# Kernel tuning notes

Hardware: AMD Instinct MI355X
Metric: run time of the kernel (lower is better)

Reference implementation:

```python
import jax, jax.numpy as jnp
import numpy as np

DXV, DRUGV = 10000, 3000
DXANC, DRUGANC = 2000, 600
A = 8            # max ancestors per leaf
ONTOD = 128; EHRD = 128; ATTND = 128; PTATTND = 128; DPL = 500
B, T, DXN, DRUGN = 64, 20, 30, 30


def _l2norm(x):
    n = jnp.sqrt(jnp.sum(x * x, axis=-1, keepdims=True))
    return x / jnp.maximum(n, 1e-12)


def _onto_emb(emb, leaves, ancestors, aW, ab, cW, cb):
    # GRAM-style ontology attention: per leaf, attend over its ancestor set.
    le = emb[leaves]          # (V, A, ONTOD)
    ae = emb[ancestors]       # (V, A, ONTOD)
    s = jnp.tanh(jnp.concatenate([le, ae], -1) @ aW + ab) @ cW + cb  # (V, A, 1)
    attn = jax.nn.softmax(s, axis=1)
    out = jnp.sum(attn * ae, axis=1)                                 # (V, ONTOD)
    pad = jnp.zeros((1, out.shape[1]), out.dtype)                    # padding row at idx V
    return jnp.concatenate([out, pad], axis=0)


def setup_inputs() -> dict:
    key = jax.random.key(0)
    ks = jax.random.split(key, 24)
    s = 0.02
    dxseqs = jax.random.randint(ks[0], (B, T, DXN), 0, DXV + 1)
    drugseqs = jax.random.randint(ks[1], (B, T, DRUGN), 0, DRUGV + 1)
    dx_onehot = jax.random.uniform(ks[2], (T, B, DXV), dtype=jnp.float32)
    drug_onehot = jax.random.uniform(ks[3], (T, B, DRUGV), dtype=jnp.float32)
    dx_leaves = jnp.broadcast_to(jnp.arange(DXV)[:, None], (DXV, A))
    dx_ancestors = jax.random.randint(ks[4], (DXV, A), 0, DXV + DXANC).at[:, 0].set(jnp.arange(DXV))
    drug_leaves = jnp.broadcast_to(jnp.arange(DRUGV)[:, None], (DRUGV, A))
    drug_ancestors = jax.random.randint(ks[5], (DRUGV, A), 0, DRUGV + DRUGANC).at[:, 0].set(jnp.arange(DRUGV))
    ehr_dx_emb = (jax.random.normal(ks[6], (DXV + 1, EHRD)) * s).at[DXV].set(0.0)
    ehr_drug_emb = (jax.random.normal(ks[7], (DRUGV + 1, EHRD)) * s).at[DRUGV].set(0.0)
    return {
        "dxseqs": dxseqs, "drugseqs": drugseqs,
        "dx_onehot": dx_onehot, "drug_onehot": drug_onehot,
        "dx_leaves": dx_leaves, "dx_ancestors": dx_ancestors,
        "drug_leaves": drug_leaves, "drug_ancestors": drug_ancestors,
        "dx_onto_emb": jax.random.normal(ks[8], (DXV + DXANC, ONTOD)) * s,
        "dx_onto_aW": jax.random.normal(ks[9], (2 * ONTOD, ATTND)) * s,
        "dx_onto_ab": jnp.zeros((ATTND,)),
        "dx_onto_cW": jax.random.normal(ks[10], (ATTND, 1)) * s,
        "dx_onto_cb": jnp.zeros((1,)),
        "drug_onto_emb": jax.random.normal(ks[11], (DRUGV + DRUGANC, ONTOD)) * s,
        "drug_onto_aW": jax.random.normal(ks[12], (2 * ONTOD, ATTND)) * s,
        "drug_onto_ab": jnp.zeros((ATTND,)),
        "drug_onto_cW": jax.random.normal(ks[13], (ATTND, 1)) * s,
        "drug_onto_cb": jnp.zeros((1,)),
        "ehr_dx_emb": ehr_dx_emb, "ehr_drug_emb": ehr_drug_emb,
        "co_W": jax.random.normal(ks[14], (EHRD, DXV + DRUGV)) * s,
        "co_b": jnp.zeros((DXV + DRUGV,)),
        "attn_W": jax.random.normal(ks[15], (2 * ONTOD + 2 * EHRD, PTATTND)) * s,
        "attn_b": jnp.zeros((PTATTND,)),
        "comb_W": jax.random.normal(ks[16], (PTATTND, 1)) * s,
        "comb_b": jnp.zeros((1,)),
        "dp_W": jax.random.normal(ks[17], (ONTOD + EHRD, DPL)) * s,
        "dp_b": jnp.zeros((DPL,)),
        "read_W": jax.random.normal(ks[18], (ONTOD + EHRD, 1)) * s,
        "read_b": jnp.zeros((1,)),
    }


def reference(dxseqs, drugseqs, dx_onehot, drug_onehot,
              dx_leaves, dx_ancestors, drug_leaves, drug_ancestors,
              dx_onto_emb, dx_onto_aW, dx_onto_ab, dx_onto_cW, dx_onto_cb,
              drug_onto_emb, drug_onto_aW, drug_onto_ab, drug_onto_cW, drug_onto_cb,
              ehr_dx_emb, ehr_drug_emb, co_W, co_b,
              attn_W, attn_b, comb_W, comb_b, dp_W, dp_b, read_W, read_b):
    dxALL = _onto_emb(dx_onto_emb, dx_leaves, dx_ancestors, dx_onto_aW, dx_onto_ab, dx_onto_cW, dx_onto_cb)      # (DXV+1, ONTOD)
    drugALL = _onto_emb(drug_onto_emb, drug_leaves, drug_ancestors, drug_onto_aW, drug_onto_ab, drug_onto_cW, drug_onto_cb)
    dxE = ehr_dx_emb[dxseqs]                                # (B,T,DXN,EHRD)
    drugE = ehr_drug_emb[drugseqs]                          # (B,T,DRUGN,EHRD)
    EHREmb = jnp.concatenate([dxE, drugE], axis=2)          # (B,T,N,EHRD)
    ontoEmb = jnp.concatenate([dxALL[dxseqs], drugALL[drugseqs]], axis=2)  # (B,T,N,ONTOD)
    EHRVEmb = _l2norm(jnp.sum(dxE, axis=2)) + _l2norm(jnp.sum(drugE, axis=2))  # (B,T,EHRD)
    dxontoV = jnp.einsum('tbv,vd->btd', dx_onehot, dxALL[:-1])
    drugontoV = jnp.einsum('tbv,vd->btd', drug_onehot, drugALL[:-1])
    cooccurU = jax.nn.softmax(EHRVEmb @ co_W + co_b, axis=2)               # (B,T,DXV+DRUGV)
    vonehot = jnp.concatenate([jnp.transpose(dx_onehot, (1, 0, 2)),
                               jnp.transpose(drug_onehot, (1, 0, 2))], axis=2)
    cooccur_loss = -jnp.mean(jnp.sum(vonehot * jnp.log(cooccurU), axis=(1, 2)))
    ontoV = _l2norm(dxontoV) + _l2norm(drugontoV)
    vs = jnp.concatenate([ontoV, EHRVEmb], axis=2)          # (B,T,ONTOD+EHRD)
    dxdrug = jnp.concatenate([EHREmb, ontoEmb], axis=3)     # (B,T,N,EHRD+ONTOD)
    N = dxdrug.shape[2]
    vs_rep = jnp.broadcast_to(vs[:, :, None, :], (vs.shape[0], vs.shape[1], N, vs.shape[2]))
    attnInput = jnp.concatenate([vs_rep, dxdrug], axis=3)   # (B,T,N,2*ONTOD+2*EHRD)
    pre = jnp.tanh(attnInput @ attn_W + attn_b) @ comb_W + comb_b          # (B,T,N,1)
    attn = jax.nn.softmax(pre, axis=2)
    vs2 = jnp.sum(attn * dxdrug, axis=2)                    # (B,T,EHRD+ONTOD)
    vs_dp = _l2norm(vs2)
    DP_result = jax.nn.softmax(jnp.tanh(vs_dp) @ dp_W + dp_b, axis=2)
    read_result = jax.nn.sigmoid(vs_dp @ read_W + read_b)
    return (read_result, DP_result, cooccur_loss * 10.0)
```

## Files before the change

kernel.cpp:

```cpp
#include <hip/hip_runtime.h>
#include <hip/hip_bf16.h>
#include <math.h>

#define BB 64
#define TT 20
#define BT 1280
#define DXV 10000
#define DRUGV 3000
#define COV 13000
#define DPL 500
#define KC 40

typedef __attribute__((ext_vector_type(8))) short short8v;
typedef __attribute__((ext_vector_type(4))) float f32x4;

__device__ __forceinline__ unsigned short f2bf(float f) {
  __hip_bfloat16 h = __float2bfloat16(f);
  return *reinterpret_cast<unsigned short*>(&h);
}

__global__ __launch_bounds__(256, 4) void k_onto(
    const float* __restrict__ emb, const int* __restrict__ leaves, const int* __restrict__ anc,
    const float* __restrict__ aW, const float* __restrict__ ab, const float* __restrict__ cW,
    float* __restrict__ out)
{
  __shared__ __align__(16) float xe[4][128];
  __shared__ __align__(16) float xa[4][8][128];
  __shared__ float part[4][8][2];
  __shared__ float sv[32];
  const int tid = threadIdx.x;
  const int v0 = blockIdx.x * 4;

  for (int i = tid; i < 4*128; i += 256) {
    const int lv = i >> 7, d = i & 127;
    xe[lv][d] = emb[leaves[(v0 + lv)*8] * 128 + d];
  }
  for (int i = tid; i < 32*128; i += 256) {
    const int row = i >> 7, d = i & 127;
    xa[row >> 3][row & 7][d] = emb[anc[(v0 + (row >> 3))*8 + (row & 7)] * 128 + d];
  }
  __syncthreads();

  const int j = tid & 127, half = tid >> 7;

  float ld[4];
  { const float abj = ab[j]; ld[0] = ld[1] = ld[2] = ld[3] = abj; }
  for (int k0 = 0; k0 < 128; k0 += 4) {
    const float w0 = aW[(k0+0)*128 + j];
    const float w1 = aW[(k0+1)*128 + j];
    const float w2 = aW[(k0+2)*128 + j];
    const float w3 = aW[(k0+3)*128 + j];
    #pragma unroll
    for (int lv = 0; lv < 4; ++lv) {
      const float4 x4 = *reinterpret_cast<const float4*>(&xe[lv][k0]);
      ld[lv] = fmaf(x4.x, w0, fmaf(x4.y, w1, fmaf(x4.z, w2, fmaf(x4.w, w3, ld[lv]))));
    }
  }

  float acc[4][4];
  #pragma unroll
  for (int lv = 0; lv < 4; ++lv)
    #pragma unroll
    for (int ai = 0; ai < 4; ++ai) acc[lv][ai] = ld[lv];
  for (int k0 = 0; k0 < 128; k0 += 4) {
    const float w0 = aW[(128+k0+0)*128 + j];
    const float w1 = aW[(128+k0+1)*128 + j];
    const float w2 = aW[(128+k0+2)*128 + j];
    const float w3 = aW[(128+k0+3)*128 + j];
    float4 es[16];
    #pragma unroll
    for (int lv = 0; lv < 4; ++lv)
      #pragma unroll
      for (int ai = 0; ai < 4; ++ai)
        es[lv*4 + ai] = *reinterpret_cast<const float4*>(&xa[lv][half + 2*ai][k0]);
    #pragma unroll
    for (int lv = 0; lv < 4; ++lv)
      #pragma unroll
      for (int ai = 0; ai < 4; ++ai) {
        const float4 e4 = es[lv*4 + ai];
        acc[lv][ai] = fmaf(e4.x, w0, fmaf(e4.y, w1, fmaf(e4.z, w2, fmaf(e4.w, w3, acc[lv][ai]))));
      }
  }

  {
    const float cwj = cW[j];
    #pragma unroll
    for (int lv = 0; lv < 4; ++lv)
      #pragma unroll
      for (int ai = 0; ai < 4; ++ai) {
        float p = tanhf(acc[lv][ai]) * cwj;
        for (int off = 32; off; off >>= 1) p += __shfl_down(p, off);
        if ((tid & 63) == 0) part[lv][half + 2*ai][(tid >> 6) & 1] = p;
      }
  }
  __syncthreads();
  if (tid < 32) sv[tid] = part[tid >> 3][tid & 7][0] + part[tid >> 3][tid & 7][1];
  __syncthreads();
  if (tid < 4) {
    float m = -1e30f;
    #pragma unroll
    for (int a = 0; a < 8; ++a) m = fmaxf(m, sv[tid*8 + a]);
    float e[8], ssum = 0.f;
    #pragma unroll
    for (int a = 0; a < 8; ++a) { e[a] = __expf(sv[tid*8 + a] - m); ssum += e[a]; }
    const float inv = 1.f / ssum;
    #pragma unroll
    for (int a = 0; a < 8; ++a) sv[tid*8 + a] = e[a] * inv;
  }
  __syncthreads();
  #pragma unroll
  for (int it = 0; it < 2; ++it) {
    const int i = it*256 + tid;
    const int lv = i >> 7, d = i & 127;
    float o = 0.f;
    #pragma unroll
    for (int a = 0; a < 8; ++a) o += sv[lv*8 + a] * xa[lv][a][d];
    out[(v0 + lv)*128 + d] = o;
  }
}

__global__ __launch_bounds__(128) void k_ehr(
    const int* __restrict__ dxs, const int* __restrict__ drs,
    const float* __restrict__ edx, const float* __restrict__ edr,
    float* __restrict__ vs)
{
  const int bt = blockIdx.x, d = threadIdx.x;
  float sdx = 0.f, sdr = 0.f;
  for (int n = 0; n < 30; ++n) sdx += edx[dxs[bt*30 + n]*128 + d];
  for (int n = 0; n < 30; ++n) sdr += edr[drs[bt*30 + n]*128 + d];
  __shared__ float red[2][2];
  float p1 = sdx*sdx, p2 = sdr*sdr;
  for (int off = 32; off; off >>= 1) { p1 += __shfl_down(p1, off); p2 += __shfl_down(p2, off); }
  if ((d & 63) == 0) { red[0][d>>6] = p1; red[1][d>>6] = p2; }
  __syncthreads();
  const float n1 = sqrtf(red[0][0] + red[0][1]);
  const float n2 = sqrtf(red[1][0] + red[1][1]);
  vs[bt*256 + 128 + d] = sdx / fmaxf(n1, 1e-12f) + sdr / fmaxf(n2, 1e-12f);
}

__global__ __launch_bounds__(256, 4) void k_einsum(
    const float* __restrict__ oneh, const float* __restrict__ tabl,
    float* __restrict__ outp, int V, int vcount)
{
  __shared__ __align__(16) float As[32][KC];
  __shared__ __align__(16) float Bs[KC][128];
  const int tid = threadIdx.x;
  const int rbase = blockIdx.x * 32;
  const int vbase = blockIdx.y * vcount;
  const int cg = tid & 31, rg = tid >> 5;
  const int d0 = cg * 4, r0 = rg * 4;
  float acc[4][4];
  #pragma unroll
  for (int r = 0; r < 4; ++r)
    #pragma unroll
    for (int q = 0; q < 4; ++q) acc[r][q] = 0.f;

  for (int c0 = 0; c0 < vcount; c0 += KC) {
    __syncthreads();
    for (int i = tid; i < 320; i += 256) {
      const int r = i / 10, q = i % 10;
      const int row = rbase + r;
      const int b = row / TT, t = row % TT;
      *reinterpret_cast<float4*>(&As[r][q*4]) =
          *reinterpret_cast<const float4*>(&oneh[(t*BB + b)*V + vbase + c0 + q*4]);
    }
    for (int i = tid; i < 1280; i += 256) {
      const int rr = i >> 5, q = i & 31;
      *reinterpret_cast<float4*>(&Bs[rr][q*4]) =
          *reinterpret_cast<const float4*>(&tabl[(vbase + c0 + rr)*128 + q*4]);
    }
    __syncthreads();
    #pragma unroll
    for (int kk = 0; kk < KC; kk += 4) {
      const float4 b0 = *reinterpret_cast<const float4*>(&Bs[kk+0][d0]);
      const float4 b1 = *reinterpret_cast<const float4*>(&Bs[kk+1][d0]);
      const float4 b2 = *reinterpret_cast<const float4*>(&Bs[kk+2][d0]);
      const float4 b3 = *reinterpret_cast<const float4*>(&Bs[kk+3][d0]);
      float4 a4[4];
      #pragma unroll
      for (int r = 0; r < 4; ++r) a4[r] = *reinterpret_cast<const float4*>(&As[r0 + r][kk]);
      #pragma unroll
      for (int r = 0; r < 4; ++r) {
        acc[r][0] = fmaf(a4[r].x, b0.x, fmaf(a4[r].y, b1.x, fmaf(a4[r].z, b2.x, fmaf(a4[r].w, b3.x, acc[r][0]))));
        acc[r][1] = fmaf(a4[r].x, b0.y, fmaf(a4[r].y, b1.y, fmaf(a4[r].z, b2.y, fmaf(a4[r].w, b3.y, acc[r][1]))));
        acc[r][2] = fmaf(a4[r].x, b0.z, fmaf(a4[r].y, b1.z, fmaf(a4[r].z, b2.z, fmaf(a4[r].w, b3.z, acc[r][2]))));
        acc[r][3] = fmaf(a4[r].x, b0.w, fmaf(a4[r].y, b1.w, fmaf(a4[r].z, b2.w, fmaf(a4[r].w, b3.w, acc[r][3]))));
      }
    }
  }
  #pragma unroll
  for (int r = 0; r < 4; ++r) {
    const int row = rbase + r0 + r;
    #pragma unroll
    for (int q = 0; q < 4; ++q)
      atomicAdd(&outp[row*128 + d0 + q], acc[r][q]);
  }
}

__global__ __launch_bounds__(128) void k_vs(
    const float* __restrict__ dxo, const float* __restrict__ dro, float* __restrict__ vs)
{
  const int bt = blockIdx.x, d = threadIdx.x;
  const float a = dxo[bt*128 + d], b = dro[bt*128 + d];
  __shared__ float red[2][2];
  float p1 = a*a, p2 = b*b;
  for (int off = 32; off; off >>= 1) { p1 += __shfl_down(p1, off); p2 += __shfl_down(p2, off); }
  if ((d & 63) == 0) { red[0][d>>6] = p1; red[1][d>>6] = p2; }
  __syncthreads();
  const float n1 = sqrtf(red[0][0] + red[0][1]);
  const float n2 = sqrtf(red[1][0] + red[1][1]);
  vs[bt*256 + d] = a / fmaxf(n1, 1e-12f) + b / fmaxf(n2, 1e-12f);
}

__global__ __launch_bounds__(256, 4) void k_cooc(
    const float* __restrict__ vs, const float* __restrict__ coW, const float* __restrict__ cob,
    const float* __restrict__ dxoh, const float* __restrict__ droh,
    float* __restrict__ es_g, float* __restrict__ od_g, float* __restrict__ os_g)
{
  __shared__ __align__(16) float ev[16][128];
  __shared__ float l_es[16], l_od[16], l_os[16];
  const int tid = threadIdx.x;
  const int rbase = blockIdx.x * 16;
  const int cbase = blockIdx.y * 512;
  for (int i = tid; i < 2048; i += 256)
    ev[i >> 7][i & 127] = vs[(rbase + (i >> 7))*256 + 128 + (i & 127)];
  if (tid < 16) { l_es[tid] = 0.f; l_od[tid] = 0.f; l_os[tid] = 0.f; }
  __syncthreads();
  float es[16], od[16], os[16];
  #pragma unroll
  for (int r = 0; r < 16; ++r) { es[r] = 0.f; od[r] = 0.f; os[r] = 0.f; }
  #pragma unroll 1
  for (int vi = 0; vi < 2; ++vi) {
    const int v = cbase + vi*256 + tid;
    if (v < COV) {
      float acc[16];
      #pragma unroll
      for (int r = 0; r < 16; ++r) acc[r] = 0.f;
      for (int k0 = 0; k0 < 128; k0 += 4) {
        const float c0 = coW[(k0+0)*COV + v];
        const float c1 = coW[(k0+1)*COV + v];
        const float c2 = coW[(k0+2)*COV + v];
        const float c3 = coW[(k0+3)*COV + v];
        float4 e4s[16];
        #pragma unroll
        for (int r = 0; r < 16; ++r) e4s[r] = *reinterpret_cast<const float4*>(&ev[r][k0]);
        #pragma unroll
        for (int r = 0; r < 16; ++r)
          acc[r] = fmaf(e4s[r].x, c0, fmaf(e4s[r].y, c1, fmaf(e4s[r].z, c2, fmaf(e4s[r].w, c3, acc[r]))));
      }
      const float cb = cob[v];
      #pragma unroll
      for (int r = 0; r < 16; ++r) {
        const int row = rbase + r;
        const int b = row / TT, t = row % TT;
        const float lgv = acc[r] + cb;
        const float oh = (v < DXV) ? dxoh[(t*BB + b)*DXV + v]
                                   : droh[(t*BB + b)*DRUGV + (v - DXV)];
        es[r] += __expf(lgv);
        od[r] = fmaf(oh, lgv, od[r]);
        os[r] += oh;
      }
    }
  }
  #pragma unroll
  for (int r = 0; r < 16; ++r) {
    float a = es[r], b2 = od[r], c2 = os[r];
    for (int off = 32; off; off >>= 1) {
      a += __shfl_down(a, off); b2 += __shfl_down(b2, off); c2 += __shfl_down(c2, off);
    }
    if ((tid & 63) == 0) { atomicAdd(&l_es[r], a); atomicAdd(&l_od[r], b2); atomicAdd(&l_os[r], c2); }
  }
  __syncthreads();
  if (tid < 16) {
    atomicAdd(&es_g[rbase + tid], l_es[tid]);
    atomicAdd(&od_g[rbase + tid], l_od[tid]);
    atomicAdd(&os_g[rbase + tid], l_os[tid]);
  }
}

__global__ __launch_bounds__(256) void k_loss(
    const float* __restrict__ es_g, const float* __restrict__ od_g, const float* __restrict__ os_g,
    float* __restrict__ out)
{
  const int tid = threadIdx.x;
  float a = 0.f;
  for (int r = tid; r < BT; r += 256)
    a += logf(es_g[r]) * os_g[r] - od_g[r];
  __shared__ float red[4];
  for (int off = 32; off; off >>= 1) a += __shfl_down(a, off);
  if ((tid & 63) == 0) red[tid >> 6] = a;
  __syncthreads();
  if (tid == 0) out[0] = (red[0] + red[1] + red[2] + red[3]) * (10.f / (float)BB);
}

__global__ __launch_bounds__(128) void k_cvtw(
    const float* __restrict__ aW, unsigned short* __restrict__ aWbT)
{
  const int k = blockIdx.x, n = threadIdx.x;
  aWbT[n*256 + k] = f2bf(aW[(256 + k)*128 + n]);
}

__global__ __launch_bounds__(256, 4) void k_attn(
    const int* __restrict__ dxs, const int* __restrict__ drs,
    const float* __restrict__ edx, const float* __restrict__ edr,
    const float* __restrict__ dxALL, const float* __restrict__ drugALL,
    const float* __restrict__ vs, const float* __restrict__ aW,
    const float* __restrict__ ab, const float* __restrict__ cWc,
    const unsigned short* __restrict__ aWbT,
    float* __restrict__ vsdp)
{
  __shared__ __align__(16) unsigned short X2[64*256];
  __shared__ __align__(16) float vrow[256];
  __shared__ float bp[2][128];
  __shared__ float base[128];
  __shared__ float sattn[64];
  __shared__ int codes[60];
  __shared__ float red[4];
  const int tid = threadIdx.x;
  const int bt = blockIdx.x;
  char* x2b = reinterpret_cast<char*>(X2);

  if (tid < 64) sattn[tid] = 0.f;
  if (tid < 60) codes[tid] = (tid < 30) ? dxs[bt*30 + tid] : drs[bt*30 + tid - 30];
  vrow[tid] = vs[bt*256 + tid];
  __syncthreads();

  for (int idx = tid; idx < 60*64; idx += 256) {
    const int n = idx >> 6, q = idx & 63;
    const float* src = (q < 32) ? ((n < 30) ? edx : edr)
                                : ((n < 30) ? dxALL : drugALL);
    const float4 v = *reinterpret_cast<const float4*>(&src[codes[n]*128 + (q & 31)*4]);
    ushort4 h;
    h.x = f2bf(v.x); h.y = f2bf(v.y); h.z = f2bf(v.z); h.w = f2bf(v.w);
    const int byte = (n*512 + q*8) ^ ((n & 7) << 4);
    *reinterpret_cast<ushort4*>(x2b + byte) = h;
  }
  for (int idx = tid; idx < 4*64; idx += 256) {
    const int n = 60 + (idx >> 6), q = idx & 63;
    *reinterpret_cast<ushort4*>(x2b + ((n*512 + q*8) ^ ((n & 7) << 4))) = ushort4{0,0,0,0};
  }

  const int j = tid & 127, ng = tid >> 7;
  {
    float p = 0.f;
    const int kb = ng * 128;
    for (int k0 = 0; k0 < 128; k0 += 4) {
      const float4 v4 = *reinterpret_cast<const float4*>(&vrow[kb + k0]);
      p = fmaf(v4.x, aW[(kb+k0+0)*128 + j],
          fmaf(v4.y, aW[(kb+k0+1)*128 + j],
          fmaf(v4.z, aW[(kb+k0+2)*128 + j],
          fmaf(v4.w, aW[(kb+k0+3)*128 + j], p))));
    }
    bp[ng][j] = p;
  }
  __syncthreads();
  if (tid < 128) base[tid] = ab[tid] + bp[0][tid] + bp[1][tid];
  __syncthreads();

  const int lane = tid & 63, w = tid >> 6;
  const int l15 = lane & 15, kg = lane >> 4;
  f32x4 acc[4][2];
  #pragma unroll
  for (int mt = 0; mt < 4; ++mt)
    #pragma unroll
    for (int ns = 0; ns < 2; ++ns) acc[mt][ns] = f32x4{0.f, 0.f, 0.f, 0.f};

  #pragma unroll
  for (int kt = 0; kt < 8; ++kt) {
    short8v a[4];
    #pragma unroll
    for (int mt = 0; mt < 4; ++mt) {
      const int row = mt*16 + l15;
      const int byte = (row*512 + kt*64 + kg*16) ^ ((row & 7) << 4);
      a[mt] = *reinterpret_cast<const short8v*>(x2b + byte);
    }
    #pragma unroll
    for (int ns = 0; ns < 2; ++ns) {
      const int ncol = (2*w + ns)*16 + l15;
      const short8v b = *reinterpret_cast<const short8v*>(
          reinterpret_cast<const char*>(aWbT) + ncol*512 + kt*64 + kg*16);
      #pragma unroll
      for (int mt = 0; mt < 4; ++mt)
        acc[mt][ns] = __builtin_amdgcn_mfma_f32_16x16x32_bf16(a[mt], b, acc[mt][ns], 0, 0, 0);
    }
  }

  {
    const int c0 = 2*w*16 + l15, c1 = c0 + 16;
    const float b0 = base[c0], b1 = base[c1];
    const float cw0 = cWc[c0], cw1 = cWc[c1];
    #pragma unroll
    for (int mt = 0; mt < 4; ++mt) {
      #pragma unroll
      for (int r = 0; r < 4; ++r) {
        float p = fmaf(cw0, tanhf(b0 + acc[mt][0][r]), cw1 * tanhf(b1 + acc[mt][1][r]));
        p += __shfl_xor(p, 1); p += __shfl_xor(p, 2);
        p += __shfl_xor(p, 4); p += __shfl_xor(p, 8);
        const int row = mt*16 + kg*4 + r;
        if (l15 == 0 && row < 60) atomicAdd(&sattn[row], p);
      }
    }
  }
  __syncthreads();

  if (tid < 64) {
    const float v = (tid < 60) ? sattn[tid] : -1e30f;
    float m = v;
    for (int off = 32; off; off >>= 1) m = fmaxf(m, __shfl_xor(m, off));
    const float e = (tid < 60) ? __expf(v - m) : 0.f;
    float s = e;
    for (int off = 32; off; off >>= 1) s += __shfl_xor(s, off);
    if (tid < 60) sattn[tid] = e / s;
  }
  __syncthreads();

  float acc2 = 0.f;
  {
    const int d2 = tid * 2;
    for (int n = 0; n < 60; ++n) {
      const unsigned short u = *reinterpret_cast<const unsigned short*>(
          x2b + ((n*512 + d2) ^ ((n & 7) << 4)));
      acc2 = fmaf(sattn[n], __uint_as_float(((unsigned)u) << 16), acc2);
    }
  }
  float p = acc2 * acc2;
  for (int off = 32; off; off >>= 1) p += __shfl_down(p, off);
  if ((tid & 63) == 0) red[tid >> 6] = p;
  __syncthreads();
  const float nrm = sqrtf(red[0] + red[1] + red[2] + red[3]);
  vsdp[bt*256 + tid] = acc2 / fmaxf(nrm, 1e-12f);
}

__global__ __launch_bounds__(256) void k_out(
    const float* __restrict__ vsdp, const float* __restrict__ dpW, const float* __restrict__ dpb,
    const float* __restrict__ rW, const float* __restrict__ rb, float* __restrict__ out)
{
  __shared__ __align__(16) float tv[256];
  __shared__ float lg[512];
  __shared__ float red[4], red2[4], red3[4];
  const int bt = blockIdx.x, tid = threadIdx.x;
  const float vraw = vsdp[bt*256 + tid];
  tv[tid] = tanhf(vraw);
  __syncthreads();
  for (int l = tid; l < DPL; l += 256) {
    float a = dpb[l];
    for (int k0 = 0; k0 < 256; k0 += 4) {
      const float4 t4 = *reinterpret_cast<const float4*>(&tv[k0]);
      a = fmaf(t4.x, dpW[(k0+0)*DPL + l],
          fmaf(t4.y, dpW[(k0+1)*DPL + l],
          fmaf(t4.z, dpW[(k0+2)*DPL + l],
          fmaf(t4.w, dpW[(k0+3)*DPL + l], a))));
    }
    lg[l] = a;
  }
  __syncthreads();
  float m = -1e30f;
  for (int l = tid; l < DPL; l += 256) m = fmaxf(m, lg[l]);
  for (int off = 32; off; off >>= 1) m = fmaxf(m, __shfl_xor(m, off));
  if ((tid & 63) == 0) red[tid >> 6] = m;
  __syncthreads();
  m = fmaxf(fmaxf(red[0], red[1]), fmaxf(red[2], red[3]));
  float s = 0.f;
  for (int l = tid; l < DPL; l += 256) s += __expf(lg[l] - m);
  for (int off = 32; off; off >>= 1) s += __shfl_xor(s, off);
  if ((tid & 63) == 0) red2[tid >> 6] = s;
  __syncthreads();
  s = red2[0] + red2[1] + red2[2] + red2[3];
  const float inv = 1.f / s;
  for (int l = tid; l < DPL; l += 256) out[BT + bt*DPL + l] = __expf(lg[l] - m) * inv;
  float p = vraw * rW[tid];
  for (int off = 32; off; off >>= 1) p += __shfl_down(p, off);
  if ((tid & 63) == 0) red3[tid >> 6] = p;
  __syncthreads();
  if (tid == 0) {
    const float tot = red3[0] + red3[1] + red3[2] + red3[3] + rb[0];
    out[bt] = 1.f / (1.f + __expf(-tot));
  }
}

extern "C" void kernel_launch(void* const* d_in, const int* in_sizes, int n_in,
                              void* d_out, int out_size, void* d_ws, size_t ws_size,
                              hipStream_t stream) {
  const int*   dxseqs = (const int*)d_in[0];
  const int*   drseqs = (const int*)d_in[1];
  const float* dxoh   = (const float*)d_in[2];
  const float* droh   = (const float*)d_in[3];
  const int*   dxlv   = (const int*)d_in[4];
  const int*   dxan   = (const int*)d_in[5];
  const int*   drlv   = (const int*)d_in[6];
  const int*   dran   = (const int*)d_in[7];
  const float* dxoe   = (const float*)d_in[8];
  const float* dxaW   = (const float*)d_in[9];
  const float* dxab   = (const float*)d_in[10];
  const float* dxcW   = (const float*)d_in[11];
  const float* droe   = (const float*)d_in[13];
  const float* draW   = (const float*)d_in[14];
  const float* drab   = (const float*)d_in[15];
  const float* drcW   = (const float*)d_in[16];
  const float* edx    = (const float*)d_in[18];
  const float* edr    = (const float*)d_in[19];
  const float* coW    = (const float*)d_in[20];
  const float* cob    = (const float*)d_in[21];
  const float* aW     = (const float*)d_in[22];
  const float* ab     = (const float*)d_in[23];
  const float* cWc    = (const float*)d_in[24];
  const float* dpW    = (const float*)d_in[26];
  const float* dpb    = (const float*)d_in[27];
  const float* rW     = (const float*)d_in[28];
  const float* rb     = (const float*)d_in[29];
  float* out = (float*)d_out;

  float* ws      = (float*)d_ws;
  float* dxALL   = ws;
  float* drugALL = dxALL   + 10001*128;
  float* vsbuf   = drugALL + 3001*128;
  float* dxoV    = vsbuf   + 1280*256;
  float* droV    = dxoV    + 1280*128;
  float* vsdp    = droV    + 1280*128;
  float* es_g    = vsdp    + 1280*256;
  float* od_g    = es_g    + 1280;
  float* os_g    = od_g    + 1280;
  unsigned short* aWbT = (unsigned short*)(os_g + 1280);

  hipMemsetAsync(dxALL + 10000*128, 0, 128*sizeof(float), stream);
  hipMemsetAsync(drugALL + 3000*128, 0, 128*sizeof(float), stream);
  hipMemsetAsync(dxoV, 0, 2*1280*128*sizeof(float), stream);
  hipMemsetAsync(es_g, 0, 3*1280*sizeof(float), stream);

  k_cvtw<<<256, 128, 0, stream>>>(aW, aWbT);
  k_onto<<<DXV/4,  256, 0, stream>>>(dxoe, dxlv, dxan, dxaW, dxab, dxcW, dxALL);
  k_onto<<<DRUGV/4,256, 0, stream>>>(droe, drlv, dran, draW, drab, drcW, drugALL);
  k_ehr<<<BT, 128, 0, stream>>>(dxseqs, drseqs, edx, edr, vsbuf);
  k_einsum<<<dim3(BT/32, 10), 256, 0, stream>>>(dxoh, dxALL, dxoV, DXV, 1000);
  k_einsum<<<dim3(BT/32, 5),  256, 0, stream>>>(droh, drugALL, droV, DRUGV, 600);
  k_vs<<<BT, 128, 0, stream>>>(dxoV, droV, vsbuf);
  k_cooc<<<dim3(BT/16, 26), 256, 0, stream>>>(vsbuf, coW, cob, dxoh, droh, es_g, od_g, os_g);
  k_loss<<<1, 256, 0, stream>>>(es_g, od_g, os_g, out + BT + BT*DPL);
  k_attn<<<BT, 256, 0, stream>>>(dxseqs, drseqs, edx, edr, dxALL, drugALL, vsbuf, aW, ab, cWc, aWbT, vsdp);
  k_out<<<BT, 256, 0, stream>>>(vsdp, dpW, dpb, rW, rb, out);
}
```

Measured before the change: 652.9 us.

## Use bf16 MFMA for co-occurrence logits with pre-transposed bf16 weights

```diff
diff --git a/kernel.cpp b/kernel.cpp
--- a/kernel.cpp
+++ b/kernel.cpp
@@ -212,66 +212,110 @@
   vs[bt*256 + d] = a / fmaxf(n1, 1e-12f) + b / fmaxf(n2, 1e-12f);
 }
 
+__global__ __launch_bounds__(256) void k_cvtco(
+    const float* __restrict__ coW, unsigned short* __restrict__ coWbT)
+{
+  __shared__ float t[32][129];
+  const int v0 = blockIdx.x * 32;
+  const int tid = threadIdx.x;
+  for (int i = tid; i < 128*32; i += 256) {
+    const int k = i >> 5, v = i & 31;
+    if (v0 + v < COV) t[v][k] = coW[k*COV + v0 + v];
+  }
+  __syncthreads();
+  for (int i = tid; i < 32*128; i += 256) {
+    const int v = i >> 7, k = i & 127;
+    if (v0 + v < COV) coWbT[(v0 + v)*128 + k] = f2bf(t[v][k]);
+  }
+}
+
 __global__ __launch_bounds__(256, 4) void k_cooc(
-    const float* __restrict__ vs, const float* __restrict__ coW, const float* __restrict__ cob,
+    const float* __restrict__ vs, const unsigned short* __restrict__ coWbT,
+    const float* __restrict__ cob,
     const float* __restrict__ dxoh, const float* __restrict__ droh,
     float* __restrict__ es_g, float* __restrict__ od_g, float* __restrict__ os_g)
 {
-  __shared__ __align__(16) float ev[16][128];
-  __shared__ float l_es[16], l_od[16], l_os[16];
+  __shared__ __align__(16) unsigned short Xa[32*128];
+  __shared__ float l_es[32], l_od[32], l_os[32];
   const int tid = threadIdx.x;
-  const int rbase = blockIdx.x * 16;
-  const int cbase = blockIdx.y * 512;
-  for (int i = tid; i < 2048; i += 256)
-    ev[i >> 7][i & 127] = vs[(rbase + (i >> 7))*256 + 128 + (i & 127)];
-  if (tid < 16) { l_es[tid] = 0.f; l_od[tid] = 0.f; l_os[tid] = 0.f; }
-  __syncthreads();
-  float es[16], od[16], os[16];
-  #pragma unroll
-  for (int r = 0; r < 16; ++r) { es[r] = 0.f; od[r] = 0.f; os[r] = 0.f; }
-  #pragma unroll 1
-  for (int vi = 0; vi < 2; ++vi) {
-    const int v = cbase + vi*256 + tid;
-    if (v < COV) {
-      float acc[16];
-      #pragma unroll
-      for (int r = 0; r < 16; ++r) acc[r] = 0.f;
-      for (int k0 = 0; k0 < 128; k0 += 4) {
-        const float c0 = coW[(k0+0)*COV + v];
-        const float c1 = coW[(k0+1)*COV + v];
-        const float c2 = coW[(k0+2)*COV + v];
-        const float c3 = coW[(k0+3)*COV + v];
-        float4 e4s[16];
-        #pragma unroll
-        for (int r = 0; r < 16; ++r) e4s[r] = *reinterpret_cast<const float4*>(&ev[r][k0]);
-        #pragma unroll
-        for (int r = 0; r < 16; ++r)
-          acc[r] = fmaf(e4s[r].x, c0, fmaf(e4s[r].y, c1, fmaf(e4s[r].z, c2, fmaf(e4s[r].w, c3, acc[r]))));
-      }
-      const float cb = cob[v];
-      #pragma unroll
-      for (int r = 0; r < 16; ++r) {
-        const int row = rbase + r;
-        const int b = row / TT, t = row % TT;
-        const float lgv = acc[r] + cb;
-        const float oh = (v < DXV) ? dxoh[(t*BB + b)*DXV + v]
-                                   : droh[(t*BB + b)*DRUGV + (v - DXV)];
-        es[r] += __expf(lgv);
-        od[r] = fmaf(oh, lgv, od[r]);
-        os[r] += oh;
-      }
-    }
-  }
-  #pragma unroll
-  for (int r = 0; r < 16; ++r) {
-    float a = es[r], b2 = od[r], c2 = os[r];
-    for (int off = 32; off; off >>= 1) {
-      a += __shfl_down(a, off); b2 += __shfl_down(b2, off); c2 += __shfl_down(c2, off);
-    }
-    if ((tid & 63) == 0) { atomicAdd(&l_es[r], a); atomicAdd(&l_od[r], b2); atomicAdd(&l_os[r], c2); }
-  }
-  __syncthreads();
-  if (tid < 16) {
+  const int rbase = blockIdx.x * 32;
+  const int nbase = blockIdx.y * 512;
+  char* xb = reinterpret_cast<char*>(Xa);
+
+  if (tid < 32) { l_es[tid] = 0.f; l_od[tid] = 0.f; l_os[tid] = 0.f; }
+  for (int i = tid; i < 32*32; i += 256) {
+    const int r = i >> 5, q = i & 31;
+    const float4 v = *reinterpret_cast<const float4*>(&vs[(rbase + r)*256 + 128 + q*4]);
+    ushort4 h;
+    h.x = f2bf(v.x); h.y = f2bf(v.y); h.z = f2bf(v.z); h.w = f2bf(v.w);
+    const int byte = (r*256 + q*8) ^ ((r & 7) << 4);
+    *reinterpret_cast<ushort4*>(xb + byte) = h;
+  }
+  __syncthreads();
+
+  const int lane = tid & 63, w = tid >> 6;
+  const int l15 = lane & 15, kg = lane >> 4;
+  const int nw = nbase + w*128;
+  f32x4 acc[2][8];
+  #pragma unroll
+  for (int mt = 0; mt < 2; ++mt)
+    #pragma unroll
+    for (int nt = 0; nt < 8; ++nt) acc[mt][nt] = f32x4{0.f, 0.f, 0.f, 0.f};
+
+  #pragma unroll
+  for (int kt = 0; kt < 4; ++kt) {
+    short8v a[2];
+    #pragma unroll
+    for (int mt = 0; mt < 2; ++mt) {
+      const int row = mt*16 + l15;
+      a[mt] = *reinterpret_cast<const short8v*>(xb + ((row*256 + kt*64 + kg*16) ^ ((row & 7) << 4)));
+    }
+    #pragma unroll
+    for (int nt = 0; nt < 8; ++nt) {
+      int ncol = nw + nt*16 + l15;
+      if (ncol > COV - 1) ncol = COV - 1;
+      const short8v b = *reinterpret_cast<const short8v*>(
+          reinterpret_cast<const char*>(coWbT) + ncol*256 + kt*64 + kg*16);
+      acc[0][nt] = __builtin_amdgcn_mfma_f32_16x16x32_bf16(a[0], b, acc[0][nt], 0, 0, 0);
+      acc[1][nt] = __builtin_amdgcn_mfma_f32_16x16x32_bf16(a[1], b, acc[1][nt], 0, 0, 0);
+    }
+  }
+
+  #pragma unroll
+  for (int mt = 0; mt < 2; ++mt) {
+    #pragma unroll
+    for (int r = 0; r < 4; ++r) {
+      const int lrow = mt*16 + kg*4 + r;
+      const int grow = rbase + lrow;
+      const int b_ = grow / TT, t_ = grow % TT;
+      float es_a = 0.f, od_a = 0.f, os_a = 0.f;
+      #pragma unroll
+      for (int nt = 0; nt < 8; ++nt) {
+        const int v = nw + nt*16 + l15;
+        if (v < COV) {
+          const float lgv = acc[mt][nt][r] + cob[v];
+          const float oh = (v < DXV) ? dxoh[(t_*BB + b_)*DXV + v]
+                                     : droh[(t_*BB + b_)*DRUGV + (v - DXV)];
+          es_a += __expf(lgv);
+          od_a = fmaf(oh, lgv, od_a);
+          os_a += oh;
+        }
+      }
+      #pragma unroll
+      for (int off = 1; off < 16; off <<= 1) {
+        es_a += __shfl_xor(es_a, off);
+        od_a += __shfl_xor(od_a, off);
+        os_a += __shfl_xor(os_a, off);
+      }
+      if (l15 == 0) {
+        atomicAdd(&l_es[lrow], es_a);
+        atomicAdd(&l_od[lrow], od_a);
+        atomicAdd(&l_os[lrow], os_a);
+      }
+    }
+  }
+  __syncthreads();
+  if (tid < 32) {
     atomicAdd(&es_g[rbase + tid], l_es[tid]);
     atomicAdd(&od_g[rbase + tid], l_od[tid]);
     atomicAdd(&os_g[rbase + tid], l_os[tid]);
@@ -520,7 +564,8 @@
   float* es_g    = vsdp    + 1280*256;
   float* od_g    = es_g    + 1280;
   float* os_g    = od_g    + 1280;
-  unsigned short* aWbT = (unsigned short*)(os_g + 1280);
+  unsigned short* aWbT  = (unsigned short*)(os_g + 1280);
+  unsigned short* coWbT = aWbT + 128*256;
 
   hipMemsetAsync(dxALL + 10000*128, 0, 128*sizeof(float), stream);
   hipMemsetAsync(drugALL + 3000*128, 0, 128*sizeof(float), stream);
@@ -528,13 +573,14 @@
   hipMemsetAsync(es_g, 0, 3*1280*sizeof(float), stream);
 
   k_cvtw<<<256, 128, 0, stream>>>(aW, aWbT);
+  k_cvtco<<<(COV + 31)/32, 256, 0, stream>>>(coW, coWbT);
   k_onto<<<DXV/4,  256, 0, stream>>>(dxoe, dxlv, dxan, dxaW, dxab, dxcW, dxALL);
   k_onto<<<DRUGV/4,256, 0, stream>>>(droe, drlv, dran, draW, drab, drcW, drugALL);
   k_ehr<<<BT, 128, 0, stream>>>(dxseqs, drseqs, edx, edr, vsbuf);
   k_einsum<<<dim3(BT/32, 10), 256, 0, stream>>>(dxoh, dxALL, dxoV, DXV, 1000);
   k_einsum<<<dim3(BT/32, 5),  256, 0, stream>>>(droh, drugALL, droV, DRUGV, 600);
   k_vs<<<BT, 128, 0, stream>>>(dxoV, droV, vsbuf);
-  k_cooc<<<dim3(BT/16, 26), 256, 0, stream>>>(vsbuf, coW, cob, dxoh, droh, es_g, od_g, os_g);
+  k_cooc<<<dim3(BT/32, 26), 256, 0, stream>>>(vsbuf, coWbT, cob, dxoh, droh, es_g, od_g, os_g);
   k_loss<<<1, 256, 0, stream>>>(es_g, od_g, os_g, out + BT + BT*DPL);
   k_attn<<<BT, 256, 0, stream>>>(dxseqs, drseqs, edx, edr, dxALL, drugALL, vsbuf, aW, ab, cWc, aWbT, vsdp);
   k_out<<<BT, 256, 0, stream>>>(vsdp, dpW, dpb, rW, rb, out);
```

Result: faster. 608.1 us (-6.9%).
